# Kernel optimization log

Hardware: AMD Instinct MI355X
Metric: run time of the kernel (lower is better)

## Reference

```python
import jax, jax.numpy as jnp
import numpy as np

TOKENS = 1024
IN_W = 512
BLOCK = 256
OUT_W = 512
N_BLOCKS = 64
K = 2


def setup_inputs() -> dict:
    key = jax.random.key(0)
    ks = jax.random.split(key, 8)
    u = lambda k, s: jax.random.uniform(k, s, jnp.float32, -1.0, 1.0)
    return {
        "x": jax.random.normal(ks[0], (TOKENS, IN_W), jnp.float32),
        "noise": jax.random.normal(ks[1], (TOKENS, N_BLOCKS), jnp.float32),
        "w1s": u(ks[2], (N_BLOCKS, IN_W, BLOCK)),
        "b1s": u(ks[3], (N_BLOCKS, BLOCK)),
        "w2s": u(ks[4], (N_BLOCKS, BLOCK, OUT_W)),
        "b2s": u(ks[5], (N_BLOCKS, OUT_W)),
        "mixer": jnp.zeros((IN_W, N_BLOCKS), jnp.float32) + 0.01 * jax.random.normal(ks[6], (IN_W, N_BLOCKS), jnp.float32),
        "noise_controller": jnp.zeros((IN_W, N_BLOCKS), jnp.float32) + 0.01 * jax.random.normal(ks[7], (IN_W, N_BLOCKS), jnp.float32),
        "k": K,
    }


def reference(x, noise, w1s, b1s, w2s, b2s, mixer, noise_controller, k):
    # noisy routing logits: mixer_prod + randn * softplus(noise_prod)
    h_x = x @ mixer + noise * jax.nn.softplus(x @ noise_controller)  # [B, E]
    topk_vals, topk_idx = jax.lax.top_k(h_x, k)                       # [B, K]
    scores = jax.nn.softmax(topk_vals, axis=-1)                       # [B, K]
    # per-token expert weight gather (faithful to index_select semantics)
    gw1 = w1s[topk_idx]  # [B, K, I, H]
    gb1 = b1s[topk_idx]  # [B, K, H]
    gw2 = w2s[topk_idx]  # [B, K, H, O]
    gb2 = b2s[topk_idx]  # [B, K, O]
    v = jax.nn.relu(jnp.einsum('bi,bkih->bkh', x, gw1) + gb1)        # [B, K, H]
    out = jnp.einsum('bkh,bkho->bko', v, gw2) + gb2                   # [B, K, O]
    return jnp.sum(out * scores[..., None], axis=1)                   # [B, O]
```

## Files before the change

### kernel.cpp

```cpp
#include <hip/hip_runtime.h>
#include <math.h>

#define TOKENS    1024
#define IN_W      512
#define BLOCK_H   256
#define OUT_W     512
#define N_EXPERTS 64
#define TOPK      2
#define NSLOTS    (TOKENS * TOPK)
#define LIST_CAP  128
#define T_CAP     12
#define NGRP      4
#define XPAD      520
#define VPAD      264

__global__ __launch_bounds__(256) void routing_kernel(
    const float* __restrict__ x, const float* __restrict__ noise,
    const float* __restrict__ mixer, const float* __restrict__ noisec,
    float* __restrict__ esc, int* __restrict__ counts, int* __restrict__ lists,
    float* __restrict__ out)
{
    __shared__ float xs[2 * 512];
    __shared__ float pm[2 * 2 * 64];
    __shared__ float pn[2 * 2 * 64];
    const int blk  = blockIdx.x;
    const int tid  = threadIdx.x;
    const int wave = tid >> 6, lane = tid & 63;
    const int tq = wave >> 1;
    const int ih = wave & 1;

    ((float4*)xs)[tid] = ((const float4*)x)[(size_t)blk * 256 + tid];
    ((float4*)(out + (size_t)blk * 2 * OUT_W))[tid] = make_float4(0.f, 0.f, 0.f, 0.f);
    __syncthreads();

    float am = 0.f, an = 0.f;
    const float* xp = xs + tq * 512 + ih * 256;
    const float* mp = mixer  + (size_t)(ih * 256) * 64 + lane;
    const float* np = noisec + (size_t)(ih * 256) * 64 + lane;
    #pragma unroll 8
    for (int i = 0; i < 256; ++i) {
        const float xv = xp[i];
        am = fmaf(xv, mp[i * 64], am);
        an = fmaf(xv, np[i * 64], an);
    }
    pm[tq * 128 + ih * 64 + lane] = am;
    pn[tq * 128 + ih * 64 + lane] = an;
    __syncthreads();

    if (tid < 128) {
        const int e = tid & 63, tt = tid >> 6;
        const int t = blk * 2 + tt;
        const float am2 = pm[tt * 128 + e] + pm[tt * 128 + 64 + e];
        const float an2 = pn[tt * 128 + e] + pn[tt * 128 + 64 + e];
        const float sp = fmaxf(an2, 0.f) + log1pf(expf(-fabsf(an2)));
        pm[tt * 128 + e] = am2 + noise[(size_t)t * 64 + e] * sp;
    }
    __syncthreads();

    if (tid < 2) {
        const float* h = pm + tid * 128;
        float b0 = -INFINITY, b1 = -INFINITY;
        int i0 = 0, i1 = 0;
        for (int i = 0; i < N_EXPERTS; ++i) {
            const float v = h[i];
            if (v > b0)      { b1 = b0; i1 = i0; b0 = v; i0 = i; }
            else if (v > b1) { b1 = v; i1 = i; }
        }
        const float z   = expf(b1 - b0);
        const float inv = 1.f / (1.f + z);
        const int t = blk * 2 + tid;
        esc[t * 2 + 0] = inv;
        esc[t * 2 + 1] = z * inv;
        const int p0 = atomicAdd(&counts[i0], 1);
        if (p0 < LIST_CAP) lists[i0 * LIST_CAP + p0] = t * 2 + 0;
        const int p1 = atomicAdd(&counts[i1], 1);
        if (p1 < LIST_CAP) lists[i1 * LIST_CAP + p1] = t * 2 + 1;
    }
}

__device__ __forceinline__ void red_xor(float4& v, int m) {
    v.x += __shfl_xor(v.x, m); v.y += __shfl_xor(v.y, m);
    v.z += __shfl_xor(v.z, m); v.w += __shfl_xor(v.w, m);
}

template<int T>
__device__ __forceinline__ void run_pass(
    int nTok, int wave, int lane,
    const float4* __restrict__ w1v, const float4* __restrict__ w2v,
    const float4* __restrict__ b1v, const float4* __restrict__ b2v,
    const float* __restrict__ xs, float* __restrict__ vsm,
    const int* __restrict__ slotIds, const float* __restrict__ escv,
    float* __restrict__ out)
{
    {
        const int c4l = lane & 3, r0 = lane >> 2;
        float4 acc[T];
        #pragma unroll
        for (int t = 0; t < T; ++t) acc[t] = make_float4(0.f, 0.f, 0.f, 0.f);
        const float4* wp = w1v + (size_t)(r0 * 64 + wave * 4 + c4l);
        const float*  xb = xs + r0;
        #pragma unroll 4
        for (int s = 0; s < 32; ++s) {
            const float4 w = wp[(size_t)s * 1024];
            #pragma unroll
            for (int t = 0; t < T; ++t) {
                const float xv = xb[t * XPAD + s * 16];
                acc[t].x = fmaf(xv, w.x, acc[t].x);
                acc[t].y = fmaf(xv, w.y, acc[t].y);
                acc[t].z = fmaf(xv, w.z, acc[t].z);
                acc[t].w = fmaf(xv, w.w, acc[t].w);
            }
        }
        #pragma unroll
        for (int t = 0; t < T; ++t) {
            red_xor(acc[t], 4); red_xor(acc[t], 8);
            red_xor(acc[t], 16); red_xor(acc[t], 32);
        }
        if (r0 == 0) {
            const float4 bb = b1v[wave * 4 + c4l];
            #pragma unroll
            for (int t = 0; t < T; ++t) {
                float4 r;
                r.x = fmaxf(acc[t].x + bb.x, 0.f);
                r.y = fmaxf(acc[t].y + bb.y, 0.f);
                r.z = fmaxf(acc[t].z + bb.z, 0.f);
                r.w = fmaxf(acc[t].w + bb.w, 0.f);
                *(float4*)&vsm[t * VPAD + wave * 16 + c4l * 4] = r;
            }
        }
    }
    __syncthreads();

    {
        const int c8 = lane & 7, r8 = lane >> 3;
        float4 acc[T];
        #pragma unroll
        for (int t = 0; t < T; ++t) acc[t] = make_float4(0.f, 0.f, 0.f, 0.f);
        const float4* wp = w2v + (size_t)(r8 * 128 + wave * 8 + c8);
        const float*  vb = vsm + r8;
        #pragma unroll 4
        for (int s = 0; s < 32; ++s) {
            const float4 w = wp[(size_t)s * 1024];
            #pragma unroll
            for (int t = 0; t < T; ++t) {
                const float vv = vb[t * VPAD + s * 8];
                acc[t].x = fmaf(vv, w.x, acc[t].x);
                acc[t].y = fmaf(vv, w.y, acc[t].y);
                acc[t].z = fmaf(vv, w.z, acc[t].z);
                acc[t].w = fmaf(vv, w.w, acc[t].w);
            }
        }
        #pragma unroll
        for (int t = 0; t < T; ++t) {
            red_xor(acc[t], 8); red_xor(acc[t], 16); red_xor(acc[t], 32);
        }
        const float4 bb = b2v[wave * 8 + c8];
        #pragma unroll
        for (int t = 0; t < T; ++t) {
            if ((t & 7) == r8 && t < nTok) {
                const float sc = escv[t];
                float* o = out + (size_t)(slotIds[t] >> 1) * OUT_W
                               + (wave * 8 + c8) * 4;
                atomicAdd(o + 0, (acc[t].x + bb.x) * sc);
                atomicAdd(o + 1, (acc[t].y + bb.y) * sc);
                atomicAdd(o + 2, (acc[t].z + bb.z) * sc);
                atomicAdd(o + 3, (acc[t].w + bb.w) * sc);
            }
        }
    }
}

__global__ __launch_bounds__(1024, 4) void expert_kernel(
    const float* __restrict__ x,
    const float* __restrict__ w1s, const float* __restrict__ b1s,
    const float* __restrict__ w2s, const float* __restrict__ b2s,
    const int* __restrict__ counts, const int* __restrict__ lists,
    const float* __restrict__ esc, float* __restrict__ out)
{
    __shared__ __align__(16) float xs[T_CAP * XPAD];
    __shared__ __align__(16) float vsm[T_CAP * VPAD];
    __shared__ int   slotIds[T_CAP];
    __shared__ float escv[T_CAP];

    const int e  = blockIdx.x;
    const int g  = blockIdx.y;
    const int ne = min(counts[e], LIST_CAP);
    const int tid  = threadIdx.x;
    const int wave = tid >> 6, lane = tid & 63;

    const float4* w1v = (const float4*)(w1s + (size_t)e * IN_W * BLOCK_H);
    const float4* w2v = (const float4*)(w2s + (size_t)e * BLOCK_H * OUT_W);
    const float4* b1v = (const float4*)(b1s + (size_t)e * BLOCK_H);
    const float4* b2v = (const float4*)(b2s + (size_t)e * OUT_W);
    const float4* x4  = (const float4*)x;

    for (int s0 = g; s0 < ne; s0 += NGRP * T_CAP) {
        const int nTok  = min(T_CAP, (ne - s0 + NGRP - 1) / NGRP);
        const int Tpath = (nTok <= 4) ? 4 : (nTok <= 8) ? 8 : 12;

        if (tid < T_CAP) {
            int s = 0; float sc = 0.f;
            if (tid < nTok) { s = lists[e * LIST_CAP + s0 + tid * NGRP]; sc = esc[s]; }
            slotIds[tid] = s;
            escv[tid]    = sc;
        }
        __syncthreads();

        for (int idx = tid; idx < Tpath * 128; idx += 1024) {
            const int t = idx >> 7, q = idx & 127;
            float4 v = make_float4(0.f, 0.f, 0.f, 0.f);
            if (t < nTok) v = x4[(size_t)(slotIds[t] >> 1) * 128 + q];
            *(float4*)&xs[t * XPAD + q * 4] = v;
        }
        __syncthreads();

        if (nTok <= 4)
            run_pass<4>(nTok, wave, lane, w1v, w2v, b1v, b2v, xs, vsm, slotIds, escv, out);
        else if (nTok <= 8)
            run_pass<8>(nTok, wave, lane, w1v, w2v, b1v, b2v, xs, vsm, slotIds, escv, out);
        else
            run_pass<12>(nTok, wave, lane, w1v, w2v, b1v, b2v, xs, vsm, slotIds, escv, out);
        __syncthreads();
    }
}

extern "C" void kernel_launch(void* const* d_in, const int* in_sizes, int n_in,
                              void* d_out, int out_size, void* d_ws, size_t ws_size,
                              hipStream_t stream) {
    const float* x      = (const float*)d_in[0];
    const float* noise  = (const float*)d_in[1];
    const float* w1s    = (const float*)d_in[2];
    const float* b1s    = (const float*)d_in[3];
    const float* w2s    = (const float*)d_in[4];
    const float* b2s    = (const float*)d_in[5];
    const float* mixer  = (const float*)d_in[6];
    const float* noisec = (const float*)d_in[7];
    float* out = (float*)d_out;

    char* ws = (char*)d_ws;
    int*   counts = (int*)ws;                       ws += 256;
    float* esc    = (float*)ws;                     ws += NSLOTS * sizeof(float);
    int*   lists  = (int*)ws;

    hipMemsetAsync(counts, 0, 256, stream);

    routing_kernel<<<TOKENS / 2, 256, 0, stream>>>(x, noise, mixer, noisec,
                                                   esc, counts, lists, out);
    expert_kernel<<<dim3(N_EXPERTS, NGRP), 1024, 0, stream>>>(
        x, w1s, b1s, w2s, b2s, counts, lists, esc, out);
}
```

Baseline: 186.1 us.

## Stream expert weights through double-buffered LDS with async global-to-LDS loads

Expert weight tiles (W1, then W2) now go through a double-buffered 64KB LDS staging area. The copies use global_load_lds with an XOR swizzle, and each chunk is prefetched while the previous one is computed. The first W2 chunk is staged during the last W1 iteration. The goal is to hide the latency of direct strided global loads of weights. In exchange it adds a block-wide barrier every chunk, extra LDS traffic, and a larger LDS footprint that may lower occupancy. The padding on the x and v tiles is removed.

```diff
diff --git a/kernel.cpp b/kernel.cpp
--- a/kernel.cpp
+++ b/kernel.cpp
@@ -11,8 +11,13 @@
 #define LIST_CAP  128
 #define T_CAP     12
 #define NGRP      4
-#define XPAD      520
-#define VPAD      264
+#define XPAD      512
+#define VPAD      256
+
+#define WCHUNK_BYTES  32768
+#define WCHUNK_FLOATS 8192
+#define W1_NCHUNK     16
+#define W2_NCHUNK     16
 
 __global__ __launch_bounds__(256) void routing_kernel(
     const float* __restrict__ x, const float* __restrict__ noise,
@@ -83,33 +88,77 @@
     v.z += __shfl_xor(v.z, m); v.w += __shfl_xor(v.w, m);
 }
 
+__device__ __forceinline__ void fma4(float4& a, float s, const float4& w) {
+    a.x = fmaf(s, w.x, a.x); a.y = fmaf(s, w.y, a.y);
+    a.z = fmaf(s, w.z, a.z); a.w = fmaf(s, w.w, a.w);
+}
+
+__device__ __forceinline__ void stage_w1(const char* w1e, float* wlds, int buf,
+                                         int k, int wave, int lane) {
+    const char* gbase = w1e + (size_t)k * 32 * 1024;
+    #pragma unroll
+    for (int rr = 0; rr < 2; ++rr) {
+        const int o  = rr * 16384 + wave * 1024 + lane * 16;
+        const int r  = o >> 10;
+        const int cs = (o >> 4) & 63;
+        const int c  = cs ^ (r & 7);
+        const char* g = gbase + r * 1024 + c * 16;
+        float* l = wlds + (size_t)buf * WCHUNK_FLOATS + (rr * 16384 + wave * 1024) / 4;
+        __builtin_amdgcn_global_load_lds(
+            (const __attribute__((address_space(1))) void*)g,
+            (__attribute__((address_space(3))) void*)l, 16, 0, 0);
+    }
+}
+
+__device__ __forceinline__ void stage_w2(const char* w2e, float* wlds, int buf,
+                                         int k, int wave, int lane) {
+    const char* gbase = w2e + (size_t)k * 16 * 2048;
+    #pragma unroll
+    for (int rr = 0; rr < 2; ++rr) {
+        const int o  = rr * 16384 + wave * 1024 + lane * 16;
+        const int r  = o >> 11;
+        const int cs = (o >> 4) & 127;
+        const int c  = cs ^ (r & 7);
+        const char* g = gbase + r * 2048 + c * 16;
+        float* l = wlds + (size_t)buf * WCHUNK_FLOATS + (rr * 16384 + wave * 1024) / 4;
+        __builtin_amdgcn_global_load_lds(
+            (const __attribute__((address_space(1))) void*)g,
+            (__attribute__((address_space(3))) void*)l, 16, 0, 0);
+    }
+}
+
 template<int T>
 __device__ __forceinline__ void run_pass(
     int nTok, int wave, int lane,
-    const float4* __restrict__ w1v, const float4* __restrict__ w2v,
+    const char* w1e, const char* w2e,
     const float4* __restrict__ b1v, const float4* __restrict__ b2v,
-    const float* __restrict__ xs, float* __restrict__ vsm,
+    const float* __restrict__ xs, float* __restrict__ vsm, float* __restrict__ wlds,
     const int* __restrict__ slotIds, const float* __restrict__ escv,
     float* __restrict__ out)
 {
+    const int c4l = lane & 3, r0 = lane >> 2;
+    const int c8  = lane & 7, r8 = lane >> 3;
+
     {
-        const int c4l = lane & 3, r0 = lane >> 2;
         float4 acc[T];
         #pragma unroll
         for (int t = 0; t < T; ++t) acc[t] = make_float4(0.f, 0.f, 0.f, 0.f);
-        const float4* wp = w1v + (size_t)(r0 * 64 + wave * 4 + c4l);
-        const float*  xb = xs + r0;
-        #pragma unroll 4
-        for (int s = 0; s < 32; ++s) {
-            const float4 w = wp[(size_t)s * 1024];
+        const int swz = ((wave * 4 + c4l) ^ (r0 & 7)) * 4;
+        const float* xb = xs + r0;
+        for (int k = 0; k < W1_NCHUNK; ++k) {
+            if (k + 1 < W1_NCHUNK) stage_w1(w1e, wlds, (k + 1) & 1, k + 1, wave, lane);
+            else                   stage_w2(w2e, wlds, 0, 0, wave, lane);
+            const float* wb = wlds + (k & 1) * WCHUNK_FLOATS;
+            const float4 wA = *(const float4*)&wb[r0 * 256 + swz];
+            const float4 wB = *(const float4*)&wb[(r0 + 16) * 256 + swz];
             #pragma unroll
             for (int t = 0; t < T; ++t) {
-                const float xv = xb[t * XPAD + s * 16];
-                acc[t].x = fmaf(xv, w.x, acc[t].x);
-                acc[t].y = fmaf(xv, w.y, acc[t].y);
-                acc[t].z = fmaf(xv, w.z, acc[t].z);
-                acc[t].w = fmaf(xv, w.w, acc[t].w);
+                const float xvA = xb[t * XPAD + k * 32];
+                const float xvB = xb[t * XPAD + k * 32 + 16];
+                fma4(acc[t], xvA, wA);
+                fma4(acc[t], xvB, wB);
             }
+            __syncthreads();
         }
         #pragma unroll
         for (int t = 0; t < T; ++t) {
@@ -132,23 +181,24 @@
     __syncthreads();
 
     {
-        const int c8 = lane & 7, r8 = lane >> 3;
         float4 acc[T];
         #pragma unroll
         for (int t = 0; t < T; ++t) acc[t] = make_float4(0.f, 0.f, 0.f, 0.f);
-        const float4* wp = w2v + (size_t)(r8 * 128 + wave * 8 + c8);
-        const float*  vb = vsm + r8;
-        #pragma unroll 4
-        for (int s = 0; s < 32; ++s) {
-            const float4 w = wp[(size_t)s * 1024];
+        const int swz2 = ((wave * 8 + c8) ^ r8) * 4;
+        const float* vb = vsm + r8;
+        for (int k = 0; k < W2_NCHUNK; ++k) {
+            if (k + 1 < W2_NCHUNK) stage_w2(w2e, wlds, (k + 1) & 1, k + 1, wave, lane);
+            const float* wb = wlds + (k & 1) * WCHUNK_FLOATS;
+            const float4 wA = *(const float4*)&wb[r8 * 512 + swz2];
+            const float4 wB = *(const float4*)&wb[(r8 + 8) * 512 + swz2];
             #pragma unroll
             for (int t = 0; t < T; ++t) {
-                const float vv = vb[t * VPAD + s * 8];
-                acc[t].x = fmaf(vv, w.x, acc[t].x);
-                acc[t].y = fmaf(vv, w.y, acc[t].y);
-                acc[t].z = fmaf(vv, w.z, acc[t].z);
-                acc[t].w = fmaf(vv, w.w, acc[t].w);
+                const float vA = vb[t * VPAD + k * 16];
+                const float vB = vb[t * VPAD + k * 16 + 8];
+                fma4(acc[t], vA, wA);
+                fma4(acc[t], vB, wB);
             }
+            __syncthreads();
         }
         #pragma unroll
         for (int t = 0; t < T; ++t) {
@@ -178,6 +228,7 @@
     const float* __restrict__ esc, float* __restrict__ out)
 {
     __shared__ __align__(16) float xs[T_CAP * XPAD];
+    __shared__ __align__(16) float wlds[2 * WCHUNK_FLOATS];
     __shared__ __align__(16) float vsm[T_CAP * VPAD];
     __shared__ int   slotIds[T_CAP];
     __shared__ float escv[T_CAP];
@@ -188,8 +239,8 @@
     const int tid  = threadIdx.x;
     const int wave = tid >> 6, lane = tid & 63;
 
-    const float4* w1v = (const float4*)(w1s + (size_t)e * IN_W * BLOCK_H);
-    const float4* w2v = (const float4*)(w2s + (size_t)e * BLOCK_H * OUT_W);
+    const char* w1e = (const char*)(w1s + (size_t)e * IN_W * BLOCK_H);
+    const char* w2e = (const char*)(w2s + (size_t)e * BLOCK_H * OUT_W);
     const float4* b1v = (const float4*)(b1s + (size_t)e * BLOCK_H);
     const float4* b2v = (const float4*)(b2s + (size_t)e * OUT_W);
     const float4* x4  = (const float4*)x;
@@ -206,6 +257,7 @@
         }
         __syncthreads();
 
+        stage_w1(w1e, wlds, 0, 0, wave, lane);
         for (int idx = tid; idx < Tpath * 128; idx += 1024) {
             const int t = idx >> 7, q = idx & 127;
             float4 v = make_float4(0.f, 0.f, 0.f, 0.f);
@@ -215,11 +267,11 @@
         __syncthreads();
 
         if (nTok <= 4)
-            run_pass<4>(nTok, wave, lane, w1v, w2v, b1v, b2v, xs, vsm, slotIds, escv, out);
+            run_pass<4>(nTok, wave, lane, w1e, w2e, b1v, b2v, xs, vsm, wlds, slotIds, escv, out);
         else if (nTok <= 8)
-            run_pass<8>(nTok, wave, lane, w1v, w2v, b1v, b2v, xs, vsm, slotIds, escv, out);
+            run_pass<8>(nTok, wave, lane, w1e, w2e, b1v, b2v, xs, vsm, wlds, slotIds, escv, out);
         else
-            run_pass<12>(nTok, wave, lane, w1v, w2v, b1v, b2v, xs, vsm, slotIds, escv, out);
+            run_pass<12>(nTok, wave, lane, w1e, w2e, b1v, b2v, xs, vsm, wlds, slotIds, escv, out);
         __syncthreads();
     }
 }
```

Measured after the change: 225.5 us. +21.1%, slower.

## Stage expert weights into LDS via async global_load_lds with swizzled double buffering

Applied to the files above, without the earlier changes.

Replaces the per-thread direct global weight loads with cooperative staging of W1 and W2 column panels into shared memory through global_load_lds, using an XOR swizzle and double buffering for W2. Token inputs and hidden activations are re-laid out in LDS so each wave handles one weight slot for six tokens, reducing each dot product with full-wave shuffles. The aim is coalesced, overlapped weight traffic, at the cost of many more barriers per pass, always processing the full 12-token tile, and longer shuffle reduction chains.

```diff
diff --git a/kernel.cpp b/kernel.cpp
--- a/kernel.cpp
+++ b/kernel.cpp
@@ -11,8 +11,6 @@
 #define LIST_CAP  128
 #define T_CAP     12
 #define NGRP      4
-#define XPAD      520
-#define VPAD      264
 
 __global__ __launch_bounds__(256) void routing_kernel(
     const float* __restrict__ x, const float* __restrict__ noise,
@@ -83,90 +81,36 @@
     v.z += __shfl_xor(v.z, m); v.w += __shfl_xor(v.w, m);
 }
 
-template<int T>
-__device__ __forceinline__ void run_pass(
-    int nTok, int wave, int lane,
-    const float4* __restrict__ w1v, const float4* __restrict__ w2v,
-    const float4* __restrict__ b1v, const float4* __restrict__ b2v,
-    const float* __restrict__ xs, float* __restrict__ vsm,
-    const int* __restrict__ slotIds, const float* __restrict__ escv,
-    float* __restrict__ out)
-{
-    {
-        const int c4l = lane & 3, r0 = lane >> 2;
-        float4 acc[T];
-        #pragma unroll
-        for (int t = 0; t < T; ++t) acc[t] = make_float4(0.f, 0.f, 0.f, 0.f);
-        const float4* wp = w1v + (size_t)(r0 * 64 + wave * 4 + c4l);
-        const float*  xb = xs + r0;
-        #pragma unroll 4
-        for (int s = 0; s < 32; ++s) {
-            const float4 w = wp[(size_t)s * 1024];
-            #pragma unroll
-            for (int t = 0; t < T; ++t) {
-                const float xv = xb[t * XPAD + s * 16];
-                acc[t].x = fmaf(xv, w.x, acc[t].x);
-                acc[t].y = fmaf(xv, w.y, acc[t].y);
-                acc[t].z = fmaf(xv, w.z, acc[t].z);
-                acc[t].w = fmaf(xv, w.w, acc[t].w);
-            }
-        }
-        #pragma unroll
-        for (int t = 0; t < T; ++t) {
-            red_xor(acc[t], 4); red_xor(acc[t], 8);
-            red_xor(acc[t], 16); red_xor(acc[t], 32);
-        }
-        if (r0 == 0) {
-            const float4 bb = b1v[wave * 4 + c4l];
-            #pragma unroll
-            for (int t = 0; t < T; ++t) {
-                float4 r;
-                r.x = fmaxf(acc[t].x + bb.x, 0.f);
-                r.y = fmaxf(acc[t].y + bb.y, 0.f);
-                r.z = fmaxf(acc[t].z + bb.z, 0.f);
-                r.w = fmaxf(acc[t].w + bb.w, 0.f);
-                *(float4*)&vsm[t * VPAD + wave * 16 + c4l * 4] = r;
-            }
-        }
-    }
-    __syncthreads();
-
-    {
-        const int c8 = lane & 7, r8 = lane >> 3;
-        float4 acc[T];
-        #pragma unroll
-        for (int t = 0; t < T; ++t) acc[t] = make_float4(0.f, 0.f, 0.f, 0.f);
-        const float4* wp = w2v + (size_t)(r8 * 128 + wave * 8 + c8);
-        const float*  vb = vsm + r8;
-        #pragma unroll 4
-        for (int s = 0; s < 32; ++s) {
-            const float4 w = wp[(size_t)s * 1024];
-            #pragma unroll
-            for (int t = 0; t < T; ++t) {
-                const float vv = vb[t * VPAD + s * 8];
-                acc[t].x = fmaf(vv, w.x, acc[t].x);
-                acc[t].y = fmaf(vv, w.y, acc[t].y);
-                acc[t].z = fmaf(vv, w.z, acc[t].z);
-                acc[t].w = fmaf(vv, w.w, acc[t].w);
-            }
-        }
-        #pragma unroll
-        for (int t = 0; t < T; ++t) {
-            red_xor(acc[t], 8); red_xor(acc[t], 16); red_xor(acc[t], 32);
-        }
-        const float4 bb = b2v[wave * 8 + c8];
-        #pragma unroll
-        for (int t = 0; t < T; ++t) {
-            if ((t & 7) == r8 && t < nTok) {
-                const float sc = escv[t];
-                float* o = out + (size_t)(slotIds[t] >> 1) * OUT_W
-                               + (wave * 8 + c8) * 4;
-                atomicAdd(o + 0, (acc[t].x + bb.x) * sc);
-                atomicAdd(o + 1, (acc[t].y + bb.y) * sc);
-                atomicAdd(o + 2, (acc[t].z + bb.z) * sc);
-                atomicAdd(o + 3, (acc[t].w + bb.w) * sc);
-            }
-        }
+__device__ __forceinline__ void fma4(float4& a, float s, const float4& w) {
+    a.x = fmaf(s, w.x, a.x); a.y = fmaf(s, w.y, a.y);
+    a.z = fmaf(s, w.z, a.z); a.w = fmaf(s, w.w, a.w);
+}
+
+__device__ __forceinline__ float comp(const float4& v, int k) {
+    return k == 0 ? v.x : k == 1 ? v.y : k == 2 ? v.z : v.w;
+}
+
+__device__ __forceinline__ void stage_w1(const char* w1e, float* Wl, int p, int tid) {
+    #pragma unroll
+    for (int j = 0; j < 4; ++j) {
+        const int o  = (j * 1024 + tid) * 16;
+        const int r  = o >> 7;
+        const int c4 = ((o >> 4) & 7) ^ (r & 7);
+        __builtin_amdgcn_global_load_lds(
+            (const __attribute__((address_space(1))) void*)(w1e + (size_t)r * 1024 + p * 128 + c4 * 16),
+            (__attribute__((address_space(3))) void*)((char*)Wl + o), 16, 0, 0);
+    }
+}
+
+__device__ __forceinline__ void stage_w2(const char* w2e, float* Wl, int b, int p, int tid) {
+    #pragma unroll
+    for (int j = 0; j < 2; ++j) {
+        const int o  = (j * 1024 + tid) * 16;
+        const int r  = o >> 7;
+        const int c4 = ((o >> 4) & 7) ^ (r & 7);
+        __builtin_amdgcn_global_load_lds(
+            (const __attribute__((address_space(1))) void*)(w2e + (size_t)r * 2048 + p * 128 + c4 * 16),
+            (__attribute__((address_space(3))) void*)((char*)Wl + b * 32768 + o), 16, 0, 0);
     }
 }
 
@@ -177,8 +121,9 @@
     const int* __restrict__ counts, const int* __restrict__ lists,
     const float* __restrict__ esc, float* __restrict__ out)
 {
-    __shared__ __align__(16) float xs[T_CAP * XPAD];
-    __shared__ __align__(16) float vsm[T_CAP * VPAD];
+    __shared__ __align__(16) float Wl[16384];
+    __shared__ __align__(16) float xst[T_CAP * 512];
+    __shared__ __align__(16) float vsm[T_CAP * 256];
     __shared__ int   slotIds[T_CAP];
     __shared__ float escv[T_CAP];
 
@@ -187,16 +132,18 @@
     const int ne = min(counts[e], LIST_CAP);
     const int tid  = threadIdx.x;
     const int wave = tid >> 6, lane = tid & 63;
-
-    const float4* w1v = (const float4*)(w1s + (size_t)e * IN_W * BLOCK_H);
-    const float4* w2v = (const float4*)(w2s + (size_t)e * BLOCK_H * OUT_W);
+    const int slot = wave & 7;
+    const int tg   = wave >> 3;
+    const int wslot = slot ^ (lane & 7);
+
+    const char* w1e = (const char*)(w1s + (size_t)e * IN_W * BLOCK_H);
+    const char* w2e = (const char*)(w2s + (size_t)e * BLOCK_H * OUT_W);
     const float4* b1v = (const float4*)(b1s + (size_t)e * BLOCK_H);
     const float4* b2v = (const float4*)(b2s + (size_t)e * OUT_W);
     const float4* x4  = (const float4*)x;
 
     for (int s0 = g; s0 < ne; s0 += NGRP * T_CAP) {
-        const int nTok  = min(T_CAP, (ne - s0 + NGRP - 1) / NGRP);
-        const int Tpath = (nTok <= 4) ? 4 : (nTok <= 8) ? 8 : 12;
+        const int nTok = min(T_CAP, (ne - s0 + NGRP - 1) / NGRP);
 
         if (tid < T_CAP) {
             int s = 0; float sc = 0.f;
@@ -206,20 +153,95 @@
         }
         __syncthreads();
 
-        for (int idx = tid; idx < Tpath * 128; idx += 1024) {
+        stage_w1(w1e, Wl, 0, tid);
+        for (int idx = tid; idx < T_CAP * 128; idx += 1024) {
             const int t = idx >> 7, q = idx & 127;
             float4 v = make_float4(0.f, 0.f, 0.f, 0.f);
             if (t < nTok) v = x4[(size_t)(slotIds[t] >> 1) * 128 + q];
-            *(float4*)&xs[t * XPAD + q * 4] = v;
+            const int s = q >> 4, qm = q & 15;
+            const int base = t * 512 + (s >> 2) * 256 + 16 * qm + (s & 3);
+            xst[base +  0] = v.x;
+            xst[base +  4] = v.y;
+            xst[base +  8] = v.z;
+            xst[base + 12] = v.w;
         }
         __syncthreads();
 
-        if (nTok <= 4)
-            run_pass<4>(nTok, wave, lane, w1v, w2v, b1v, b2v, xs, vsm, slotIds, escv, out);
-        else if (nTok <= 8)
-            run_pass<8>(nTok, wave, lane, w1v, w2v, b1v, b2v, xs, vsm, slotIds, escv, out);
-        else
-            run_pass<12>(nTok, wave, lane, w1v, w2v, b1v, b2v, xs, vsm, slotIds, escv, out);
+        for (int p = 0; p < 8; ++p) {
+            float4 acc[6];
+            #pragma unroll
+            for (int t = 0; t < 6; ++t) acc[t] = make_float4(0.f, 0.f, 0.f, 0.f);
+            const float* xb = xst + (tg * 6) * 512 + lane * 4;
+            #pragma unroll
+            for (int c = 0; c < 2; ++c) {
+                float4 xv[6];
+                #pragma unroll
+                for (int t = 0; t < 6; ++t) xv[t] = *(const float4*)&xb[t * 512 + c * 256];
+                #pragma unroll
+                for (int s4 = 0; s4 < 4; ++s4) {
+                    const float4 w = *(const float4*)&Wl[((c * 4 + s4) * 64 + lane) * 32 + wslot * 4];
+                    #pragma unroll
+                    for (int t = 0; t < 6; ++t) fma4(acc[t], comp(xv[t], s4), w);
+                }
+            }
+            #pragma unroll
+            for (int t = 0; t < 6; ++t) {
+                red_xor(acc[t], 1); red_xor(acc[t], 2); red_xor(acc[t], 4);
+                red_xor(acc[t], 8); red_xor(acc[t], 16); red_xor(acc[t], 32);
+            }
+            {
+                const float4 bb = b1v[p * 8 + slot];
+                const int k = lane & 3;
+                #pragma unroll
+                for (int tt = 0; tt < 6; ++tt) {
+                    if ((lane >> 3) == tt && (lane & 4) == 0) {
+                        float av = fmaxf(comp(acc[tt], k) + comp(bb, k), 0.f);
+                        const int h = p * 32 + slot * 4 + k;
+                        vsm[(tg * 6 + tt) * 256 + (h & 63) * 4 + (h >> 6)] = av;
+                    }
+                }
+            }
+            __syncthreads();
+            if (p + 1 < 8) stage_w1(w1e, Wl, p + 1, tid);
+            else           stage_w2(w2e, Wl, 0, 0, tid);
+            __syncthreads();
+        }
+
+        for (int p = 0; p < 16; ++p) {
+            if (p + 1 < 16) stage_w2(w2e, Wl, (p + 1) & 1, p + 1, tid);
+            const float* Wb = Wl + (p & 1) * 8192;
+            float4 acc[6];
+            #pragma unroll
+            for (int t = 0; t < 6; ++t) acc[t] = make_float4(0.f, 0.f, 0.f, 0.f);
+            float4 vv[6];
+            #pragma unroll
+            for (int t = 0; t < 6; ++t) vv[t] = *(const float4*)&vsm[(tg * 6 + t) * 256 + lane * 4];
+            #pragma unroll
+            for (int s2 = 0; s2 < 4; ++s2) {
+                const float4 w = *(const float4*)&Wb[(s2 * 64 + lane) * 32 + wslot * 4];
+                #pragma unroll
+                for (int t = 0; t < 6; ++t) fma4(acc[t], comp(vv[t], s2), w);
+            }
+            #pragma unroll
+            for (int t = 0; t < 6; ++t) {
+                red_xor(acc[t], 1); red_xor(acc[t], 2); red_xor(acc[t], 4);
+                red_xor(acc[t], 8); red_xor(acc[t], 16); red_xor(acc[t], 32);
+            }
+            {
+                const float4 bb = b2v[p * 8 + slot];
+                const int k = lane & 3;
+                #pragma unroll
+                for (int tt = 0; tt < 6; ++tt) {
+                    const int t = tg * 6 + tt;
+                    if ((lane >> 3) == tt && (lane & 4) == 0 && t < nTok) {
+                        const int col = p * 32 + slot * 4 + k;
+                        atomicAdd(out + (size_t)(slotIds[t] >> 1) * OUT_W + col,
+                                  (comp(acc[tt], k) + comp(bb, k)) * escv[t]);
+                    }
+                }
+            }
+            __syncthreads();
+        }
         __syncthreads();
     }
 }
```

New measurement: 342.4 us. 1.84x slower.

## Route one token per block with float4 weight loads; lower expert unroll

Applied to the files above, without the earlier changes.

The routing kernel now handles one token per block instead of two. Each wave covers a quarter of the input rows and reads the mixer and noise-controller weights as float4, reducing them across lanes with shuffles and then across waves through shared memory. This doubles the grid to 1024 blocks and vectorises the weight loads, but every block re-reads the full mixer matrices, so total weight traffic doubles (mostly served from L2). Separately, the expert kernel's inner-loop unroll drops from 4 to 2, likely to ease register pressure.

```diff
diff --git a/kernel.cpp b/kernel.cpp
--- a/kernel.cpp
+++ b/kernel.cpp
@@ -14,61 +14,77 @@
 #define XPAD      520
 #define VPAD      264
 
+__device__ __forceinline__ void red_xor(float4& v, int m) {
+    v.x += __shfl_xor(v.x, m); v.y += __shfl_xor(v.y, m);
+    v.z += __shfl_xor(v.z, m); v.w += __shfl_xor(v.w, m);
+}
+
+__device__ __forceinline__ void fma4(float4& a, float s, const float4& w) {
+    a.x = fmaf(s, w.x, a.x); a.y = fmaf(s, w.y, a.y);
+    a.z = fmaf(s, w.z, a.z); a.w = fmaf(s, w.w, a.w);
+}
+
 __global__ __launch_bounds__(256) void routing_kernel(
     const float* __restrict__ x, const float* __restrict__ noise,
     const float* __restrict__ mixer, const float* __restrict__ noisec,
     float* __restrict__ esc, int* __restrict__ counts, int* __restrict__ lists,
     float* __restrict__ out)
 {
-    __shared__ float xs[2 * 512];
-    __shared__ float pm[2 * 2 * 64];
-    __shared__ float pn[2 * 2 * 64];
-    const int blk  = blockIdx.x;
+    __shared__ float xs[512];
+    __shared__ float pm[4 * 64];
+    __shared__ float pn[4 * 64];
+    __shared__ float hs[64];
+    const int t    = blockIdx.x;
     const int tid  = threadIdx.x;
     const int wave = tid >> 6, lane = tid & 63;
-    const int tq = wave >> 1;
-    const int ih = wave & 1;
-
-    ((float4*)xs)[tid] = ((const float4*)x)[(size_t)blk * 256 + tid];
-    ((float4*)(out + (size_t)blk * 2 * OUT_W))[tid] = make_float4(0.f, 0.f, 0.f, 0.f);
-    __syncthreads();
-
-    float am = 0.f, an = 0.f;
-    const float* xp = xs + tq * 512 + ih * 256;
-    const float* mp = mixer  + (size_t)(ih * 256) * 64 + lane;
-    const float* np = noisec + (size_t)(ih * 256) * 64 + lane;
-    #pragma unroll 8
-    for (int i = 0; i < 256; ++i) {
-        const float xv = xp[i];
-        am = fmaf(xv, mp[i * 64], am);
-        an = fmaf(xv, np[i * 64], an);
-    }
-    pm[tq * 128 + ih * 64 + lane] = am;
-    pn[tq * 128 + ih * 64 + lane] = an;
-    __syncthreads();
+    const int rs   = lane >> 4;
+    const int c    = lane & 15;
 
     if (tid < 128) {
-        const int e = tid & 63, tt = tid >> 6;
-        const int t = blk * 2 + tt;
-        const float am2 = pm[tt * 128 + e] + pm[tt * 128 + 64 + e];
-        const float an2 = pn[tt * 128 + e] + pn[tt * 128 + 64 + e];
+        ((float4*)xs)[tid] = ((const float4*)(x + (size_t)t * IN_W))[tid];
+        ((float4*)(out + (size_t)t * OUT_W))[tid] = make_float4(0.f, 0.f, 0.f, 0.f);
+    }
+    __syncthreads();
+
+    float4 am = make_float4(0.f, 0.f, 0.f, 0.f), an = am;
+    const float4* m4 = (const float4*)mixer;
+    const float4* n4 = (const float4*)noisec;
+    const int rbase = wave * 128;
+    #pragma unroll 4
+    for (int j = 0; j < 32; ++j) {
+        const int r = rbase + j * 4 + rs;
+        const float xv = xs[r];
+        const float4 wm = m4[r * 16 + c];
+        const float4 wn = n4[r * 16 + c];
+        fma4(am, xv, wm);
+        fma4(an, xv, wn);
+    }
+    red_xor(am, 16); red_xor(am, 32);
+    red_xor(an, 16); red_xor(an, 32);
+    if (lane < 16) {
+        *(float4*)&pm[wave * 64 + lane * 4] = am;
+        *(float4*)&pn[wave * 64 + lane * 4] = an;
+    }
+    __syncthreads();
+
+    if (tid < 64) {
+        const float am2 = pm[tid] + pm[64 + tid] + pm[128 + tid] + pm[192 + tid];
+        const float an2 = pn[tid] + pn[64 + tid] + pn[128 + tid] + pn[192 + tid];
         const float sp = fmaxf(an2, 0.f) + log1pf(expf(-fabsf(an2)));
-        pm[tt * 128 + e] = am2 + noise[(size_t)t * 64 + e] * sp;
-    }
-    __syncthreads();
-
-    if (tid < 2) {
-        const float* h = pm + tid * 128;
+        hs[tid] = am2 + noise[(size_t)t * 64 + tid] * sp;
+    }
+    __syncthreads();
+
+    if (tid == 0) {
         float b0 = -INFINITY, b1 = -INFINITY;
         int i0 = 0, i1 = 0;
         for (int i = 0; i < N_EXPERTS; ++i) {
-            const float v = h[i];
+            const float v = hs[i];
             if (v > b0)      { b1 = b0; i1 = i0; b0 = v; i0 = i; }
             else if (v > b1) { b1 = v; i1 = i; }
         }
         const float z   = expf(b1 - b0);
         const float inv = 1.f / (1.f + z);
-        const int t = blk * 2 + tid;
         esc[t * 2 + 0] = inv;
         esc[t * 2 + 1] = z * inv;
         const int p0 = atomicAdd(&counts[i0], 1);
@@ -76,11 +92,6 @@
         const int p1 = atomicAdd(&counts[i1], 1);
         if (p1 < LIST_CAP) lists[i1 * LIST_CAP + p1] = t * 2 + 1;
     }
-}
-
-__device__ __forceinline__ void red_xor(float4& v, int m) {
-    v.x += __shfl_xor(v.x, m); v.y += __shfl_xor(v.y, m);
-    v.z += __shfl_xor(v.z, m); v.w += __shfl_xor(v.w, m);
 }
 
 template<int T>
@@ -99,7 +110,7 @@
         for (int t = 0; t < T; ++t) acc[t] = make_float4(0.f, 0.f, 0.f, 0.f);
         const float4* wp = w1v + (size_t)(r0 * 64 + wave * 4 + c4l);
         const float*  xb = xs + r0;
-        #pragma unroll 4
+        #pragma unroll 2
         for (int s = 0; s < 32; ++s) {
             const float4 w = wp[(size_t)s * 1024];
             #pragma unroll
@@ -138,7 +149,7 @@
         for (int t = 0; t < T; ++t) acc[t] = make_float4(0.f, 0.f, 0.f, 0.f);
         const float4* wp = w2v + (size_t)(r8 * 128 + wave * 8 + c8);
         const float*  vb = vsm + r8;
-        #pragma unroll 4
+        #pragma unroll 2
         for (int s = 0; s < 32; ++s) {
             const float4 w = wp[(size_t)s * 1024];
             #pragma unroll
@@ -244,8 +255,8 @@
 
     hipMemsetAsync(counts, 0, 256, stream);
 
-    routing_kernel<<<TOKENS / 2, 256, 0, stream>>>(x, noise, mixer, noisec,
-                                                   esc, counts, lists, out);
+    routing_kernel<<<TOKENS, 256, 0, stream>>>(x, noise, mixer, noisec,
+                                               esc, counts, lists, out);
     expert_kernel<<<dim3(N_EXPERTS, NGRP), 1024, 0, stream>>>(
         x, w1s, b1s, w2s, b2s, counts, lists, esc, out);
 }
```

Result: faster. 168.8 us (-9.3%).
